# Performance work log

Measured on AMD Instinct MI355X. Metric: run time of the kernel, lower is better.

The kernel has to match this reference:

```python
import jax, jax.numpy as jnp
import numpy as np

N, E, IN, HID, H, C, NL, OUT = 50000, 500000, 384, 128, 8, 16, 3, 16
NEG_SLOPE = 0.2

def setup_inputs() -> dict:
    key = jax.random.key(0)
    ks = jax.random.split(key, 16)
    s = 0.1
    return {
        "x": jax.random.normal(ks[0], (N, IN), jnp.float32),
        "edge_index": jax.random.randint(ks[1], (2, E), 0, N, jnp.int32),
        "proj_w": jax.random.normal(ks[2], (IN, HID), jnp.float32) * s,
        "proj_b": jax.random.normal(ks[3], (HID,), jnp.float32) * s,
        "lin_w": jax.random.normal(ks[4], (NL, HID, HID), jnp.float32) * s,
        "att_src": jax.random.normal(ks[5], (NL, H, C), jnp.float32) * s,
        "att_dst": jax.random.normal(ks[6], (NL, H, C), jnp.float32) * s,
        "gat_b": jax.random.normal(ks[7], (NL, HID), jnp.float32) * s,
        "ln_g": jnp.ones((NL, HID), jnp.float32),
        "ln_b": jnp.zeros((NL, HID), jnp.float32),
        "cls_w1": jax.random.normal(ks[8], (HID, HID // 2), jnp.float32) * s,
        "cls_b1": jax.random.normal(ks[9], (HID // 2,), jnp.float32) * s,
        "cls_w2": jax.random.normal(ks[10], (HID // 2, OUT), jnp.float32) * s,
        "cls_b2": jax.random.normal(ks[11], (OUT,), jnp.float32) * s,
    }

def _layernorm(h, g, b, eps=1e-5):
    mu = jnp.mean(h, axis=-1, keepdims=True)
    var = jnp.var(h, axis=-1, keepdims=True)
    return (h - mu) * jax.lax.rsqrt(var + eps) * g + b

def _gat_layer(h, src, dst, w, a_src, a_dst, bias):
    # h: [N, HID]; per-head transform -> [N, H, C]
    xh = (h @ w).reshape(N, H, C)
    al_s = jnp.einsum('nhc,hc->nh', xh, a_src)   # [N, H]
    al_d = jnp.einsum('nhc,hc->nh', xh, a_dst)
    e = jax.nn.leaky_relu(al_s[src] + al_d[dst], NEG_SLOPE)  # [E+N, H]
    # segment softmax over incoming edges of each dst node
    m = jax.ops.segment_max(e, dst, num_segments=N)
    e = jnp.exp(e - m[dst])
    denom = jax.ops.segment_sum(e, dst, num_segments=N)
    alpha = e / (denom[dst] + 1e-16)
    msg = xh[src] * alpha[:, :, None]            # [E+N, H, C]
    out = jax.ops.segment_sum(msg, dst, num_segments=N)
    return out.reshape(N, H * C) + bias

def reference(x, edge_index, proj_w, proj_b, lin_w, att_src, att_dst, gat_b,
              ln_g, ln_b, cls_w1, cls_b1, cls_w2, cls_b2):
    loops = jnp.arange(N, dtype=edge_index.dtype)  # PyG GATConv adds self-loops
    src = jnp.concatenate([edge_index[0], loops])
    dst = jnp.concatenate([edge_index[1], loops])
    h = jax.nn.relu(x @ proj_w + proj_b)
    for l in range(NL):
        h_res = h
        h = _gat_layer(h, src, dst, lin_w[l], att_src[l], att_dst[l], gat_b[l])
        h = h + h_res
        h = jax.nn.relu(_layernorm(h, ln_g[l], ln_b[l]))
    logits = jax.nn.relu(h @ cls_w1 + cls_b1) @ cls_w2 + cls_b2
    return jax.nn.log_softmax(logits, axis=1)
```

## Files before the change

kernel.cpp:

```cpp
#include <hip/hip_runtime.h>
#include <hip/hip_bf16.h>
#include <math.h>

#define NN 50000
#define EE 500000
#define DIN 384
#define HIDD 128
#define NHEAD 8
#define OUTD 16

typedef __attribute__((ext_vector_type(8))) __bf16 bf16x8;
typedef __attribute__((ext_vector_type(4))) float f32x4;

__device__ __forceinline__ ushort f2bf(float f) {
  union { float f; unsigned u; } v; v.f = f;
  unsigned r = v.u + 0x7fffu + ((v.u >> 16) & 1u);
  return (ushort)(r >> 16);
}
__device__ __forceinline__ float bflo(unsigned w) {
  union { unsigned u; float f; } v; v.u = w << 16; return v.f;
}
__device__ __forceinline__ float bfhi(unsigned w) {
  union { unsigned u; float f; } v; v.u = w & 0xffff0000u; return v.f;
}

__global__ void zero_ints(int* p, int n) {
  int i = blockIdx.x * blockDim.x + threadIdx.x;
  if (i < n) p[i] = 0;
}

__global__ void hist_kernel(const int* __restrict__ dst, int* __restrict__ counts, int e) {
  int i = blockIdx.x * blockDim.x + threadIdx.x;
  if (i < e) atomicAdd(&counts[dst[i]], 1);
}

#define SCAN_BS 256
#define SCAN_NBLK ((NN + SCAN_BS - 1) / SCAN_BS)

__global__ __launch_bounds__(256) void partial_sums(const int* __restrict__ counts,
                                                    int* __restrict__ bsum, int n) {
  __shared__ int red[256];
  int i = blockIdx.x * 256 + threadIdx.x;
  red[threadIdx.x] = (i < n) ? counts[i] : 0;
  __syncthreads();
  #pragma unroll
  for (int off = 128; off; off >>= 1) {
    if (threadIdx.x < off) red[threadIdx.x] += red[threadIdx.x + off];
    __syncthreads();
  }
  if (threadIdx.x == 0) bsum[blockIdx.x] = red[0];
}

__global__ __launch_bounds__(256) void scan_bsums(const int* __restrict__ bsum,
                                                  int* __restrict__ boff, int nb) {
  __shared__ int buf[256];
  int t = threadIdx.x;
  int v = (t < nb) ? bsum[t] : 0;
  buf[t] = v;
  __syncthreads();
  #pragma unroll
  for (int off = 1; off < 256; off <<= 1) {
    int u = (t >= off) ? buf[t - off] : 0;
    __syncthreads();
    buf[t] += u;
    __syncthreads();
  }
  if (t < nb) boff[t] = buf[t] - v;
}

__global__ __launch_bounds__(256) void final_scan(const int* __restrict__ counts,
                                                  const int* __restrict__ boff,
                                                  int* __restrict__ rowptr,
                                                  int* __restrict__ woff, int n) {
  __shared__ int buf[256];
  int i = blockIdx.x * 256 + threadIdx.x;
  int t = threadIdx.x;
  int v = (i < n) ? counts[i] : 0;
  buf[t] = v;
  __syncthreads();
  #pragma unroll
  for (int off = 1; off < 256; off <<= 1) {
    int u = (t >= off) ? buf[t - off] : 0;
    __syncthreads();
    buf[t] += u;
    __syncthreads();
  }
  int excl = boff[blockIdx.x] + buf[t] - v;
  if (i < n) { rowptr[i] = excl; woff[i] = excl; }
  if (i == n - 1) rowptr[n] = excl + v;
}

__global__ void scatter_kernel(const int* __restrict__ src, const int* __restrict__ dst,
                               int* __restrict__ woff, int* __restrict__ col, int e) {
  int i = blockIdx.x * blockDim.x + threadIdx.x;
  if (i < e) {
    int p = atomicAdd(&woff[dst[i]], 1);
    col[p] = src[i];
  }
}

__global__ void prep_weights(const float* __restrict__ proj_w,
                             const float* __restrict__ lin_w,
                             const float* __restrict__ cls_w1,
                             const float* __restrict__ cls_w2,
                             ushort* __restrict__ wt) {
  int i = blockIdx.x * blockDim.x + threadIdx.x;
  if (i < 49152) {
    int k = i >> 7, n = i & 127;
    wt[n * 384 + k] = f2bf(proj_w[i]);
  } else if (i < 98304) {
    int j = i - 49152;
    int l = j >> 14, rem = j & 16383;
    int k = rem >> 7, n = rem & 127;
    wt[49152 + l * 16384 + n * 128 + k] = f2bf(lin_w[j]);
  } else if (i < 106496) {
    int j = i - 98304;
    int n = j >> 7, k = j & 127;
    wt[98304 + n * 128 + k] = f2bf(cls_w1[k * 64 + n]);
  } else if (i < 107520) {
    int j = i - 106496;
    int n = j >> 6, k = j & 63;
    wt[106496 + n * 64 + k] = f2bf(cls_w2[k * 16 + n]);
  }
}

#define LDS_STRIDE 72
template<typename AT, bool RELU_BIAS>
__global__ __launch_bounds__(256) void mfma_gemm64(const AT* __restrict__ A,
                                                   const ushort* __restrict__ Bt,
                                                   const float* __restrict__ bias,
                                                   ushort* __restrict__ C, int M, int K) {
  __shared__ ushort sA[64 * LDS_STRIDE];
  __shared__ ushort sB[128 * LDS_STRIDE];
  const int tid = threadIdx.x;
  const int wave = tid >> 6, lane = tid & 63;
  const int q = lane >> 4, lm = lane & 15;
  const int wr = wave >> 1, wc = wave & 1;
  const int m0 = blockIdx.x * 64;

  f32x4 acc[2][4];
  #pragma unroll
  for (int i = 0; i < 2; i++)
    #pragma unroll
    for (int j = 0; j < 4; j++) acc[i][j] = {0.f, 0.f, 0.f, 0.f};

  for (int k0 = 0; k0 < K; k0 += 64) {
    __syncthreads();
    if constexpr (sizeof(AT) == 4) {
      #pragma unroll
      for (int p = 0; p < 4; ++p) {
        int idx = p * 256 + tid;
        int r = idx >> 4;
        int c = (idx & 15) << 2;
        int row = min(m0 + r, M - 1);
        float4 v = *(const float4*)((const float*)A + (size_t)row * K + k0 + c);
        ushort4 u;
        u.x = f2bf(v.x); u.y = f2bf(v.y); u.z = f2bf(v.z); u.w = f2bf(v.w);
        *(ushort4*)&sA[r * LDS_STRIDE + c] = u;
      }
    } else {
      #pragma unroll
      for (int p = 0; p < 2; ++p) {
        int idx = p * 256 + tid;
        int r = idx >> 3;
        int c = (idx & 7) << 3;
        int row = min(m0 + r, M - 1);
        *(bf16x8*)&sA[r * LDS_STRIDE + c] =
            *(const bf16x8*)((const ushort*)A + (size_t)row * K + k0 + c);
      }
    }
    #pragma unroll
    for (int p = 0; p < 4; ++p) {
      int idx = p * 256 + tid;
      int r = idx >> 3;
      int c = (idx & 7) << 3;
      *(bf16x8*)&sB[r * LDS_STRIDE + c] = *(const bf16x8*)(Bt + (size_t)r * K + k0 + c);
    }
    __syncthreads();
    #pragma unroll
    for (int ks = 0; ks < 2; ++ks) {
      bf16x8 af[2], bfv[4];
      #pragma unroll
      for (int t = 0; t < 2; ++t)
        af[t] = *(const bf16x8*)&sA[(wr * 32 + t * 16 + lm) * LDS_STRIDE + ks * 32 + q * 8];
      #pragma unroll
      for (int t = 0; t < 4; ++t)
        bfv[t] = *(const bf16x8*)&sB[(wc * 64 + t * 16 + lm) * LDS_STRIDE + ks * 32 + q * 8];
      #pragma unroll
      for (int i = 0; i < 2; ++i)
        #pragma unroll
        for (int j = 0; j < 4; ++j)
          acc[i][j] = __builtin_amdgcn_mfma_f32_16x16x32_bf16(af[i], bfv[j], acc[i][j], 0, 0, 0);
    }
  }
  #pragma unroll
  for (int i = 0; i < 2; ++i) {
    #pragma unroll
    for (int r = 0; r < 4; ++r) {
      int row = m0 + wr * 32 + i * 16 + q * 4 + r;
      if (row < M) {
        #pragma unroll
        for (int j = 0; j < 4; ++j) {
          int colc = wc * 64 + j * 16 + lm;
          float v = acc[i][j][r];
          if (RELU_BIAS) { v += bias[colc]; v = fmaxf(v, 0.f); }
          C[(size_t)row * 128 + colc] = f2bf(v);
        }
      }
    }
  }
}

__global__ void att_logits_kernel(const ushort* __restrict__ xh,
                                  const float* __restrict__ att_s,
                                  const float* __restrict__ att_d,
                                  float* __restrict__ al_s, float* __restrict__ al_d, int n) {
  int t = blockIdx.x * blockDim.x + threadIdx.x;
  if (t >= n * NHEAD) return;
  int head = t & 7;
  const unsigned* xw = (const unsigned*)(xh + (size_t)t * 16);
  const float* as = att_s + head * 16;
  const float* ad = att_d + head * 16;
  float ss = 0.f, dd = 0.f;
  #pragma unroll
  for (int i = 0; i < 8; ++i) {
    unsigned w = xw[i];
    float x0 = bflo(w), x1 = bfhi(w);
    ss = fmaf(x0, as[i * 2], fmaf(x1, as[i * 2 + 1], ss));
    dd = fmaf(x0, ad[i * 2], fmaf(x1, ad[i * 2 + 1], dd));
  }
  al_s[t] = ss;
  al_d[t] = dd;
}

__global__ __launch_bounds__(256) void gat_aggregate(
    const ushort* __restrict__ xh, const float* __restrict__ al_s,
    const float* __restrict__ al_d, const int* __restrict__ rowptr,
    const int* __restrict__ col, const ushort* __restrict__ h_res,
    const float* __restrict__ gb, const float* __restrict__ lng,
    const float* __restrict__ lnb, ushort* __restrict__ h_out, int n) {
  const int lane = threadIdx.x & 63;
  const int node = (blockIdx.x * blockDim.x + threadIdx.x) >> 6;
  if (node >= n) return;
  const int e8 = lane >> 3;
  const int hh = lane & 7;
  const int head = lane >> 3;
  const unsigned* xw_base = (const unsigned*)xh;

  const int start = rowptr[node], end = rowptr[node + 1];
  const int T = end - start + 1;
  const float ald_c = al_d[node * 8 + hh];

  float m = -INFINITY, denom = 0.f, acc0 = 0.f, acc1 = 0.f;

  for (int c = 0; c < T; c += 8) {
    int it = c + e8;
    bool valid = it < T;
    int idx = start + it;
    int s = (valid && idx < end) ? col[idx] : node;
    float e = al_s[s * 8 + hh] + ald_c;
    e = (e > 0.f) ? e : 0.2f * e;
    if (!valid) e = -INFINITY;
    float cm = e;
    cm = fmaxf(cm, __shfl_xor(cm, 8));
    cm = fmaxf(cm, __shfl_xor(cm, 16));
    cm = fmaxf(cm, __shfl_xor(cm, 32));
    float newm = fmaxf(m, __shfl(cm, head));
    float newm_c = __shfl(newm, hh * 8);
    float p_lane = __expf(e - newm_c);
    float scale = __expf(m - newm);
    m = newm;
    unsigned xg[8];
    int sj[8];
    #pragma unroll
    for (int j = 0; j < 8; ++j) sj[j] = __shfl(s, j * 8);
    #pragma unroll
    for (int j = 0; j < 8; ++j) xg[j] = xw_base[(size_t)sj[j] * 64 + lane];
    denom *= scale; acc0 *= scale; acc1 *= scale;
    #pragma unroll
    for (int j = 0; j < 8; ++j) {
      float pj = __shfl(p_lane, j * 8 + head);
      denom += pj;
      acc0 = fmaf(pj, bflo(xg[j]), acc0);
      acc1 = fmaf(pj, bfhi(xg[j]), acc1);
    }
  }

  float inv = 1.f / denom;
  int c0 = lane * 2, c1 = c0 + 1;
  unsigned ur = ((const unsigned*)h_res)[(size_t)node * 64 + lane];
  float v0 = acc0 * inv + gb[c0] + bflo(ur);
  float v1 = acc1 * inv + gb[c1] + bfhi(ur);
  float sum = v0 + v1;
  #pragma unroll
  for (int off = 32; off; off >>= 1) sum += __shfl_xor(sum, off);
  float mean = sum * (1.f / 128.f);
  float d0 = v0 - mean, d1 = v1 - mean;
  float sq = d0 * d0 + d1 * d1;
  #pragma unroll
  for (int off = 32; off; off >>= 1) sq += __shfl_xor(sq, off);
  float rstd = rsqrtf(sq * (1.f / 128.f) + 1e-5f);
  float o0 = fmaxf(d0 * rstd * lng[c0] + lnb[c0], 0.f);
  float o1 = fmaxf(d1 * rstd * lng[c1] + lnb[c1], 0.f);
  ((unsigned*)h_out)[(size_t)node * 64 + lane] =
      (unsigned)f2bf(o0) | ((unsigned)f2bf(o1) << 16);
}

#define CSTR 136
#define HSTR 72
__global__ __launch_bounds__(256) void classifier_mfma(
    const ushort* __restrict__ h, const ushort* __restrict__ w1t,
    const float* __restrict__ b1, const ushort* __restrict__ w2t,
    const float* __restrict__ b2, float* __restrict__ out, int n) {
  __shared__ ushort sA[128 * CSTR];
  __shared__ ushort sB[64 * CSTR];
  __shared__ ushort sHid[128 * HSTR];
  const int tid = threadIdx.x;
  const int wave = tid >> 6, lane = tid & 63;
  const int q = lane >> 4, lm = lane & 15;
  const int wr = wave >> 1, wc = wave & 1;
  const int m0 = blockIdx.x * 128;

  #pragma unroll
  for (int p = 0; p < 8; ++p) {
    int idx = p * 256 + tid;
    int r = idx >> 4;
    int c = (idx & 15) << 3;
    int row = min(m0 + r, n - 1);
    *(bf16x8*)&sA[r * CSTR + c] = *(const bf16x8*)(h + (size_t)row * 128 + c);
  }
  #pragma unroll
  for (int p = 0; p < 4; ++p) {
    int idx = p * 256 + tid;
    int r = idx >> 4;
    int c = (idx & 15) << 3;
    *(bf16x8*)&sB[r * CSTR + c] = *(const bf16x8*)(w1t + r * 128 + c);
  }
  __syncthreads();

  f32x4 acc[4][2];
  #pragma unroll
  for (int i = 0; i < 4; ++i)
    #pragma unroll
    for (int j = 0; j < 2; ++j) acc[i][j] = {0.f, 0.f, 0.f, 0.f};
  #pragma unroll
  for (int ks = 0; ks < 4; ++ks) {
    bf16x8 af[4], bfv[2];
    #pragma unroll
    for (int t = 0; t < 4; ++t)
      af[t] = *(const bf16x8*)&sA[(wr * 64 + t * 16 + lm) * CSTR + ks * 32 + q * 8];
    #pragma unroll
    for (int j = 0; j < 2; ++j)
      bfv[j] = *(const bf16x8*)&sB[(wc * 32 + j * 16 + lm) * CSTR + ks * 32 + q * 8];
    #pragma unroll
    for (int i = 0; i < 4; ++i)
      #pragma unroll
      for (int j = 0; j < 2; ++j)
        acc[i][j] = __builtin_amdgcn_mfma_f32_16x16x32_bf16(af[i], bfv[j], acc[i][j], 0, 0, 0);
  }
  #pragma unroll
  for (int i = 0; i < 4; ++i) {
    #pragma unroll
    for (int j = 0; j < 2; ++j) {
      int colc = wc * 32 + j * 16 + lm;
      float bb = b1[colc];
      #pragma unroll
      for (int r = 0; r < 4; ++r) {
        int row = wr * 64 + i * 16 + q * 4 + r;
        float v = fmaxf(acc[i][j][r] + bb, 0.f);
        sHid[row * HSTR + colc] = f2bf(v);
      }
    }
  }
  __syncthreads();

  f32x4 acc2[2] = {{0.f, 0.f, 0.f, 0.f}, {0.f, 0.f, 0.f, 0.f}};
  #pragma unroll
  for (int ks = 0; ks < 2; ++ks) {
    bf16x8 b2f = *(const bf16x8*)(w2t + lm * 64 + ks * 32 + q * 8);
    #pragma unroll
    for (int t = 0; t < 2; ++t) {
      bf16x8 a2 = *(const bf16x8*)&sHid[(wave * 32 + t * 16 + lm) * HSTR + ks * 32 + q * 8];
      acc2[t] = __builtin_amdgcn_mfma_f32_16x16x32_bf16(a2, b2f, acc2[t], 0, 0, 0);
    }
  }
  float bb2 = b2[lm];
  #pragma unroll
  for (int t = 0; t < 2; ++t) {
    #pragma unroll
    for (int r = 0; r < 4; ++r) {
      int row = m0 + wave * 32 + t * 16 + q * 4 + r;
      float lg = acc2[t][r] + bb2;
      float mx = lg;
      #pragma unroll
      for (int off = 8; off; off >>= 1) mx = fmaxf(mx, __shfl_xor(mx, off, 16));
      float se = __expf(lg - mx);
      #pragma unroll
      for (int off = 8; off; off >>= 1) se += __shfl_xor(se, off, 16);
      if (row < n) out[(size_t)row * 16 + lm] = lg - mx - __logf(se);
    }
  }
}

extern "C" void kernel_launch(void* const* d_in, const int* in_sizes, int n_in,
                              void* d_out, int out_size, void* d_ws, size_t ws_size,
                              hipStream_t stream) {
  const float* x       = (const float*)d_in[0];
  const int*   ei      = (const int*)d_in[1];
  const float* proj_w  = (const float*)d_in[2];
  const float* proj_b  = (const float*)d_in[3];
  const float* lin_w   = (const float*)d_in[4];
  const float* att_src = (const float*)d_in[5];
  const float* att_dst = (const float*)d_in[6];
  const float* gat_b   = (const float*)d_in[7];
  const float* ln_g    = (const float*)d_in[8];
  const float* ln_b    = (const float*)d_in[9];
  const float* cls_w1  = (const float*)d_in[10];
  const float* cls_b1  = (const float*)d_in[11];
  const float* cls_w2  = (const float*)d_in[12];
  const float* cls_b2  = (const float*)d_in[13];
  float* outp = (float*)d_out;

  const int N = NN, E = EE;
  ushort* wt   = (ushort*)d_ws;
  ushort* h0   = wt + 108544;
  ushort* h1   = h0 + (size_t)N * 128;
  ushort* xh_u = h1 + (size_t)N * 128;
  float* als   = (float*)(xh_u + (size_t)N * 128);
  float* ald   = als + (size_t)N * NHEAD;
  int* counts  = (int*)(ald + (size_t)N * NHEAD);
  int* rowptr  = counts + N;
  int* woff    = rowptr + N + 1;
  int* col     = woff + N;
  int* bsum    = col + E;
  int* boff    = bsum + SCAN_NBLK;

  const int* e_src = ei;
  const int* e_dst = ei + E;

  prep_weights<<<(107520 + 255) / 256, 256, 0, stream>>>(proj_w, lin_w, cls_w1, cls_w2, wt);

  zero_ints<<<(N + 255) / 256, 256, 0, stream>>>(counts, N);
  hist_kernel<<<(E + 255) / 256, 256, 0, stream>>>(e_dst, counts, E);
  partial_sums<<<SCAN_NBLK, 256, 0, stream>>>(counts, bsum, N);
  scan_bsums<<<1, 256, 0, stream>>>(bsum, boff, SCAN_NBLK);
  final_scan<<<SCAN_NBLK, 256, 0, stream>>>(counts, boff, rowptr, woff, N);
  scatter_kernel<<<(E + 255) / 256, 256, 0, stream>>>(e_src, e_dst, woff, col, E);

  const int gblocks = (N + 63) / 64;
  mfma_gemm64<float, true><<<gblocks, 256, 0, stream>>>(x, wt, proj_b, h0, N, DIN);

  ushort* hc = h0;
  ushort* hn = h1;
  for (int l = 0; l < 3; ++l) {
    mfma_gemm64<ushort, false><<<gblocks, 256, 0, stream>>>(
        hc, wt + 49152 + l * 16384, nullptr, xh_u, N, 128);
    att_logits_kernel<<<(N * NHEAD + 255) / 256, 256, 0, stream>>>(
        xh_u, att_src + l * 128, att_dst + l * 128, als, ald, N);
    gat_aggregate<<<(N + 3) / 4, 256, 0, stream>>>(
        xh_u, als, ald, rowptr, col, hc, gat_b + l * 128, ln_g + l * 128,
        ln_b + l * 128, hn, N);
    ushort* t = hc; hc = hn; hn = t;
  }
  classifier_mfma<<<(N + 127) / 128, 256, 0, stream>>>(
      hc, wt + 98304, cls_b1, wt + 106496, cls_b2, outp, N);
}
```

Baseline: 381.4 us.

## Fuse attention logits into GEMM epilogue and merge setup and scan kernels

Attention logit dot products are computed in the per-layer GEMM epilogue from the fp32 accumulators via cross-lane shuffles. This removes the separate att_logits kernel and its re-read of the transformed features. The zeroing of counts is folded into the weight-prep kernel, and the block-sum scan is recomputed redundantly inside each final_scan block, which drops two launches. The epilogue adds shuffle work and register pressure to the GEMM, and the logits now come from unrounded accumulators.

Result: slower. 394.8 us (+3.5%).

```diff
diff --git a/kernel.cpp b/kernel.cpp
--- a/kernel.cpp
+++ b/kernel.cpp
@@ -24,86 +24,12 @@
   union { unsigned u; float f; } v; v.u = w & 0xffff0000u; return v.f;
 }
 
-__global__ void zero_ints(int* p, int n) {
-  int i = blockIdx.x * blockDim.x + threadIdx.x;
-  if (i < n) p[i] = 0;
-}
-
-__global__ void hist_kernel(const int* __restrict__ dst, int* __restrict__ counts, int e) {
-  int i = blockIdx.x * blockDim.x + threadIdx.x;
-  if (i < e) atomicAdd(&counts[dst[i]], 1);
-}
-
-#define SCAN_BS 256
-#define SCAN_NBLK ((NN + SCAN_BS - 1) / SCAN_BS)
-
-__global__ __launch_bounds__(256) void partial_sums(const int* __restrict__ counts,
-                                                    int* __restrict__ bsum, int n) {
-  __shared__ int red[256];
-  int i = blockIdx.x * 256 + threadIdx.x;
-  red[threadIdx.x] = (i < n) ? counts[i] : 0;
-  __syncthreads();
-  #pragma unroll
-  for (int off = 128; off; off >>= 1) {
-    if (threadIdx.x < off) red[threadIdx.x] += red[threadIdx.x + off];
-    __syncthreads();
-  }
-  if (threadIdx.x == 0) bsum[blockIdx.x] = red[0];
-}
-
-__global__ __launch_bounds__(256) void scan_bsums(const int* __restrict__ bsum,
-                                                  int* __restrict__ boff, int nb) {
-  __shared__ int buf[256];
-  int t = threadIdx.x;
-  int v = (t < nb) ? bsum[t] : 0;
-  buf[t] = v;
-  __syncthreads();
-  #pragma unroll
-  for (int off = 1; off < 256; off <<= 1) {
-    int u = (t >= off) ? buf[t - off] : 0;
-    __syncthreads();
-    buf[t] += u;
-    __syncthreads();
-  }
-  if (t < nb) boff[t] = buf[t] - v;
-}
-
-__global__ __launch_bounds__(256) void final_scan(const int* __restrict__ counts,
-                                                  const int* __restrict__ boff,
-                                                  int* __restrict__ rowptr,
-                                                  int* __restrict__ woff, int n) {
-  __shared__ int buf[256];
-  int i = blockIdx.x * 256 + threadIdx.x;
-  int t = threadIdx.x;
-  int v = (i < n) ? counts[i] : 0;
-  buf[t] = v;
-  __syncthreads();
-  #pragma unroll
-  for (int off = 1; off < 256; off <<= 1) {
-    int u = (t >= off) ? buf[t - off] : 0;
-    __syncthreads();
-    buf[t] += u;
-    __syncthreads();
-  }
-  int excl = boff[blockIdx.x] + buf[t] - v;
-  if (i < n) { rowptr[i] = excl; woff[i] = excl; }
-  if (i == n - 1) rowptr[n] = excl + v;
-}
-
-__global__ void scatter_kernel(const int* __restrict__ src, const int* __restrict__ dst,
-                               int* __restrict__ woff, int* __restrict__ col, int e) {
-  int i = blockIdx.x * blockDim.x + threadIdx.x;
-  if (i < e) {
-    int p = atomicAdd(&woff[dst[i]], 1);
-    col[p] = src[i];
-  }
-}
-
-__global__ void prep_weights(const float* __restrict__ proj_w,
+__global__ void setup_kernel(const float* __restrict__ proj_w,
                              const float* __restrict__ lin_w,
                              const float* __restrict__ cls_w1,
                              const float* __restrict__ cls_w2,
-                             ushort* __restrict__ wt) {
+                             ushort* __restrict__ wt,
+                             int* __restrict__ counts) {
   int i = blockIdx.x * blockDim.x + threadIdx.x;
   if (i < 49152) {
     int k = i >> 7, n = i & 127;
@@ -121,15 +47,87 @@
     int j = i - 106496;
     int n = j >> 6, k = j & 63;
     wt[106496 + n * 64 + k] = f2bf(cls_w2[k * 16 + n]);
+  } else {
+    int j = i - 107520;
+    if (j < NN) counts[j] = 0;
+  }
+}
+
+__global__ void hist_kernel(const int* __restrict__ dst, int* __restrict__ counts, int e) {
+  int i = blockIdx.x * blockDim.x + threadIdx.x;
+  if (i < e) atomicAdd(&counts[dst[i]], 1);
+}
+
+#define SCAN_BS 256
+#define SCAN_NBLK ((NN + SCAN_BS - 1) / SCAN_BS)
+
+__global__ __launch_bounds__(256) void partial_sums(const int* __restrict__ counts,
+                                                    int* __restrict__ bsum, int n) {
+  __shared__ int red[256];
+  int i = blockIdx.x * 256 + threadIdx.x;
+  red[threadIdx.x] = (i < n) ? counts[i] : 0;
+  __syncthreads();
+  #pragma unroll
+  for (int off = 128; off; off >>= 1) {
+    if (threadIdx.x < off) red[threadIdx.x] += red[threadIdx.x + off];
+    __syncthreads();
+  }
+  if (threadIdx.x == 0) bsum[blockIdx.x] = red[0];
+}
+
+__global__ __launch_bounds__(256) void final_scan(const int* __restrict__ counts,
+                                                  const int* __restrict__ bsum,
+                                                  int* __restrict__ rowptr,
+                                                  int* __restrict__ woff, int n, int nb) {
+  __shared__ int sb[256];
+  __shared__ int buf[256];
+  int t = threadIdx.x;
+  sb[t] = (t < nb) ? bsum[t] : 0;
+  __syncthreads();
+  #pragma unroll
+  for (int off = 1; off < 256; off <<= 1) {
+    int u = (t >= off) ? sb[t - off] : 0;
+    __syncthreads();
+    sb[t] += u;
+    __syncthreads();
+  }
+  int boffv = (blockIdx.x == 0) ? 0 : sb[blockIdx.x - 1];
+  int i = blockIdx.x * 256 + t;
+  int v = (i < n) ? counts[i] : 0;
+  buf[t] = v;
+  __syncthreads();
+  #pragma unroll
+  for (int off = 1; off < 256; off <<= 1) {
+    int u = (t >= off) ? buf[t - off] : 0;
+    __syncthreads();
+    buf[t] += u;
+    __syncthreads();
+  }
+  int excl = boffv + buf[t] - v;
+  if (i < n) { rowptr[i] = excl; woff[i] = excl; }
+  if (i == n - 1) rowptr[n] = excl + v;
+}
+
+__global__ void scatter_kernel(const int* __restrict__ src, const int* __restrict__ dst,
+                               int* __restrict__ woff, int* __restrict__ col, int e) {
+  int i = blockIdx.x * blockDim.x + threadIdx.x;
+  if (i < e) {
+    int p = atomicAdd(&woff[dst[i]], 1);
+    col[p] = src[i];
   }
 }
 
 #define LDS_STRIDE 72
-template<typename AT, bool RELU_BIAS>
+template<typename AT, bool RELU_BIAS, bool ATT>
 __global__ __launch_bounds__(256) void mfma_gemm64(const AT* __restrict__ A,
                                                    const ushort* __restrict__ Bt,
                                                    const float* __restrict__ bias,
-                                                   ushort* __restrict__ C, int M, int K) {
+                                                   ushort* __restrict__ C,
+                                                   const float* __restrict__ att_s,
+                                                   const float* __restrict__ att_d,
+                                                   float* __restrict__ al_s,
+                                                   float* __restrict__ al_d,
+                                                   int M, int K) {
   __shared__ ushort sA[64 * LDS_STRIDE];
   __shared__ ushort sB[128 * LDS_STRIDE];
   const int tid = threadIdx.x;
@@ -209,28 +207,36 @@
       }
     }
   }
-}
-
-__global__ void att_logits_kernel(const ushort* __restrict__ xh,
-                                  const float* __restrict__ att_s,
-                                  const float* __restrict__ att_d,
-                                  float* __restrict__ al_s, float* __restrict__ al_d, int n) {
-  int t = blockIdx.x * blockDim.x + threadIdx.x;
-  if (t >= n * NHEAD) return;
-  int head = t & 7;
-  const unsigned* xw = (const unsigned*)(xh + (size_t)t * 16);
-  const float* as = att_s + head * 16;
-  const float* ad = att_d + head * 16;
-  float ss = 0.f, dd = 0.f;
-  #pragma unroll
-  for (int i = 0; i < 8; ++i) {
-    unsigned w = xw[i];
-    float x0 = bflo(w), x1 = bfhi(w);
-    ss = fmaf(x0, as[i * 2], fmaf(x1, as[i * 2 + 1], ss));
-    dd = fmaf(x0, ad[i * 2], fmaf(x1, ad[i * 2 + 1], dd));
-  }
-  al_s[t] = ss;
-  al_d[t] = dd;
+  if constexpr (ATT) {
+    float as_j[4], ad_j[4];
+    #pragma unroll
+    for (int j = 0; j < 4; ++j) {
+      int head = wc * 4 + j;
+      as_j[j] = att_s[head * 16 + lm];
+      ad_j[j] = att_d[head * 16 + lm];
+    }
+    #pragma unroll
+    for (int i = 0; i < 2; ++i) {
+      #pragma unroll
+      for (int r = 0; r < 4; ++r) {
+        int row = m0 + wr * 32 + i * 16 + q * 4 + r;
+        #pragma unroll
+        for (int j = 0; j < 4; ++j) {
+          float s = acc[i][j][r] * as_j[j];
+          float d = acc[i][j][r] * ad_j[j];
+          #pragma unroll
+          for (int off = 1; off < 16; off <<= 1) {
+            s += __shfl_xor(s, off);
+            d += __shfl_xor(d, off);
+          }
+          if (lm == 0 && row < M) {
+            al_s[row * 8 + wc * 4 + j] = s;
+            al_d[row * 8 + wc * 4 + j] = d;
+          }
+        }
+      }
+    }
+  }
 }
 
 __global__ __launch_bounds__(256) void gat_aggregate(
@@ -433,30 +439,27 @@
   int* woff    = rowptr + N + 1;
   int* col     = woff + N;
   int* bsum    = col + E;
-  int* boff    = bsum + SCAN_NBLK;
 
   const int* e_src = ei;
   const int* e_dst = ei + E;
 
-  prep_weights<<<(107520 + 255) / 256, 256, 0, stream>>>(proj_w, lin_w, cls_w1, cls_w2, wt);
-
-  zero_ints<<<(N + 255) / 256, 256, 0, stream>>>(counts, N);
+  setup_kernel<<<(107520 + NN + 255) / 256, 256, 0, stream>>>(
+      proj_w, lin_w, cls_w1, cls_w2, wt, counts);
   hist_kernel<<<(E + 255) / 256, 256, 0, stream>>>(e_dst, counts, E);
   partial_sums<<<SCAN_NBLK, 256, 0, stream>>>(counts, bsum, N);
-  scan_bsums<<<1, 256, 0, stream>>>(bsum, boff, SCAN_NBLK);
-  final_scan<<<SCAN_NBLK, 256, 0, stream>>>(counts, boff, rowptr, woff, N);
+  final_scan<<<SCAN_NBLK, 256, 0, stream>>>(counts, bsum, rowptr, woff, N, SCAN_NBLK);
   scatter_kernel<<<(E + 255) / 256, 256, 0, stream>>>(e_src, e_dst, woff, col, E);
 
   const int gblocks = (N + 63) / 64;
-  mfma_gemm64<float, true><<<gblocks, 256, 0, stream>>>(x, wt, proj_b, h0, N, DIN);
+  mfma_gemm64<float, true, false><<<gblocks, 256, 0, stream>>>(
+      x, wt, proj_b, h0, nullptr, nullptr, nullptr, nullptr, N, DIN);
 
   ushort* hc = h0;
   ushort* hn = h1;
   for (int l = 0; l < 3; ++l) {
-    mfma_gemm64<ushort, false><<<gblocks, 256, 0, stream>>>(
-        hc, wt + 49152 + l * 16384, nullptr, xh_u, N, 128);
-    att_logits_kernel<<<(N * NHEAD + 255) / 256, 256, 0, stream>>>(
-        xh_u, att_src + l * 128, att_dst + l * 128, als, ald, N);
+    mfma_gemm64<ushort, false, true><<<gblocks, 256, 0, stream>>>(
+        hc, wt + 49152 + l * 16384, nullptr, xh_u,
+        att_src + l * 128, att_dst + l * 128, als, ald, N, 128);
     gat_aggregate<<<(N + 3) / 4, 256, 0, stream>>>(
         xh_u, als, ald, rowptr, col, hc, gat_b + l * 128, ln_g + l * 128,
         ln_b + l * 128, hn, N);
```
